# Performance work log

Measured on AMD Instinct MI355X. Metric: run time of the kernel, lower is better.

The kernel has to match this reference:

```python
import jax, jax.numpy as jnp
import numpy as np

B, H, N, D = 4, 8, 4096, 64
F = 64  # nb_features; must equal D because the original code multiplies k_prime (..f) elementwise with v (..d)


def setup_inputs() -> dict:
    key = jax.random.key(0)
    kq, kk, kv, kp = jax.random.split(key, 4)
    # scale inputs so exp(x @ proj.T) stays in fp32 range
    q = jax.random.normal(kq, (B, H, N, D), dtype=jnp.float32) * 0.05
    k = jax.random.normal(kk, (B, H, N, D), dtype=jnp.float32) * 0.05
    v = jax.random.normal(kv, (B, H, N, D), dtype=jnp.float32)
    proj = jax.random.normal(kp, (F, D), dtype=jnp.float32)
    return {"q": q, "k": k, "v": v, "proj": proj}


def reference(q, k, v, proj):
    # exp-kernel feature map: [b,h,n,d] x [f,d] -> [b,h,n,f]
    q_prime = jnp.exp(jnp.einsum('bhnd,fd->bhnf', q, proj))
    k_prime = jnp.exp(jnp.einsum('bhnd,fd->bhnf', k, proj))
    # denominator: sum_f q_prime * (sum_n k_prime + eps) -> [b,h,n]
    k_sum = k_prime.sum(axis=2) + 1e-6                      # [b,h,f]
    d_inv = 1.0 / jnp.einsum('bhnf,bhf->bhn', q_prime, k_sum)
    # context: elementwise product summed over sequence (requires f == d)
    ctx = (k_prime * v).sum(axis=2)                         # [b,h,d]
    out = q_prime * ctx[:, :, None, :] * d_inv[..., None]   # [b,h,n,d]
    return out
```

## Files before the change

kernel.cpp:

```cpp
#include <hip/hip_runtime.h>
#include <hip/hip_bf16.h>


#define NHEADS 32
#define SEQ    4096
#define DDIM   64

typedef __attribute__((ext_vector_type(8))) short short8;
typedef __attribute__((ext_vector_type(4))) float floatx4;

__device__ __forceinline__ short f2bf(float x) {
    unsigned int u = __float_as_uint(x);
    u += 0x7fffu + ((u >> 16) & 1u);
    return (short)(u >> 16);
}

__device__ __forceinline__ short8 load8_bf16(const float* __restrict__ p) {
    floatx4 a = *(const floatx4*)p;
    floatx4 b = *(const floatx4*)(p + 4);
    short8 t;
    t[0] = f2bf(a[0]); t[1] = f2bf(a[1]); t[2] = f2bf(a[2]); t[3] = f2bf(a[3]);
    t[4] = f2bf(b[0]); t[5] = f2bf(b[1]); t[6] = f2bf(b[2]); t[7] = f2bf(b[3]);
    return t;
}

__device__ __forceinline__ void load_bfrag(const float* __restrict__ proj,
                                           int fp, int g, short8 bfrag[4][2]) {
#pragma unroll
    for (int ft = 0; ft < 4; ++ft)
#pragma unroll
        for (int half = 0; half < 2; ++half)
            bfrag[ft][half] = load8_bf16(proj + (ft * 16 + fp) * DDIM + half * 32 + g * 8);
}

__global__ __launch_bounds__(256) void fa_pass1(const float* __restrict__ K,
                                                const float* __restrict__ V,
                                                const float* __restrict__ proj,
                                                float* __restrict__ ws) {
    const int head = blockIdx.x >> 4;
    const int seg  = blockIdx.x & 15;
    const int tid  = threadIdx.x;
    const int w    = tid >> 6;
    const int lane = tid & 63;
    const int fp   = lane & 15;
    const int g    = lane >> 4;

    short8 bfrag[4][2];
    load_bfrag(proj, fp, g, bfrag);

    float ksum[4] = {0.f, 0.f, 0.f, 0.f};
    float ctx[4]  = {0.f, 0.f, 0.f, 0.f};

    const long hbase = (long)head * SEQ;

#pragma unroll
    for (int it = 0; it < 4; ++it) {
        const int row0 = seg * 256 + it * 64 + w * 16;
        const float* ap = K + (hbase + row0 + fp) * DDIM;
        short8 afrag0 = load8_bf16(ap + g * 8);
        short8 afrag1 = load8_bf16(ap + 32 + g * 8);

        floatx4 acc[4];
#pragma unroll
        for (int ft = 0; ft < 4; ++ft) {
            floatx4 z = {0.f, 0.f, 0.f, 0.f};
            z = __builtin_amdgcn_mfma_f32_16x16x32_bf16(afrag0, bfrag[ft][0], z, 0, 0, 0);
            z = __builtin_amdgcn_mfma_f32_16x16x32_bf16(afrag1, bfrag[ft][1], z, 0, 0, 0);
            acc[ft] = z;
        }

#pragma unroll
        for (int ft = 0; ft < 4; ++ft) {
#pragma unroll
            for (int r = 0; r < 4; ++r) {
                float kp = __expf(acc[ft][r]);
                float vv = V[(hbase + row0 + g * 4 + r) * DDIM + ft * 16 + fp];
                ksum[ft] += kp;
                ctx[ft]  += kp * vv;
            }
        }
    }

#pragma unroll
    for (int ft = 0; ft < 4; ++ft) {
        ksum[ft] += __shfl_xor(ksum[ft], 16); ksum[ft] += __shfl_xor(ksum[ft], 32);
        ctx[ft]  += __shfl_xor(ctx[ft], 16);  ctx[ft]  += __shfl_xor(ctx[ft], 32);
    }

    __shared__ float red[4][128];
    if (lane < 16) {
#pragma unroll
        for (int ft = 0; ft < 4; ++ft) {
            red[w][ft * 16 + fp]      = ksum[ft];
            red[w][64 + ft * 16 + fp] = ctx[ft];
        }
    }
    __syncthreads();
    if (tid < 128) {
        float s = red[0][tid] + red[1][tid] + red[2][tid] + red[3][tid];
        atomicAdd(ws + head * 128 + tid, s);
    }
}

__global__ __launch_bounds__(256) void fa_pass2(const float* __restrict__ Q,
                                                const float* __restrict__ proj,
                                                const float* __restrict__ ws,
                                                float* __restrict__ out) {
    const int head = blockIdx.x >> 6;
    const int seg  = blockIdx.x & 63;
    const int tid  = threadIdx.x;
    const int w    = tid >> 6;
    const int lane = tid & 63;
    const int fp   = lane & 15;
    const int g    = lane >> 4;

    short8 bfrag[4][2];
    load_bfrag(proj, fp, g, bfrag);

    float ksr[4], ctxr[4];
#pragma unroll
    for (int ft = 0; ft < 4; ++ft) {
        ksr[ft]  = ws[head * 128 + ft * 16 + fp] + 1e-6f;
        ctxr[ft] = ws[head * 128 + 64 + ft * 16 + fp];
    }

    const long hbase = (long)head * SEQ;
    const int row0 = seg * 64 + w * 16;
    const float* ap = Q + (hbase + row0 + fp) * DDIM;
    short8 afrag0 = load8_bf16(ap + g * 8);
    short8 afrag1 = load8_bf16(ap + 32 + g * 8);

    float qp[4][4];
    float denom[4] = {0.f, 0.f, 0.f, 0.f};
#pragma unroll
    for (int ft = 0; ft < 4; ++ft) {
        floatx4 z = {0.f, 0.f, 0.f, 0.f};
        z = __builtin_amdgcn_mfma_f32_16x16x32_bf16(afrag0, bfrag[ft][0], z, 0, 0, 0);
        z = __builtin_amdgcn_mfma_f32_16x16x32_bf16(afrag1, bfrag[ft][1], z, 0, 0, 0);
#pragma unroll
        for (int r = 0; r < 4; ++r) {
            float e = __expf(z[r]);
            qp[ft][r] = e;
            denom[r] += e * ksr[ft];
        }
    }

#pragma unroll
    for (int r = 0; r < 4; ++r) {
        denom[r] += __shfl_xor(denom[r], 1);
        denom[r] += __shfl_xor(denom[r], 2);
        denom[r] += __shfl_xor(denom[r], 4);
        denom[r] += __shfl_xor(denom[r], 8);
        denom[r] = 1.0f / denom[r];
    }

#pragma unroll
    for (int ft = 0; ft < 4; ++ft)
#pragma unroll
        for (int r = 0; r < 4; ++r)
            out[(hbase + row0 + g * 4 + r) * DDIM + ft * 16 + fp] =
                qp[ft][r] * ctxr[ft] * denom[r];
}

extern "C" void kernel_launch(void* const* d_in, const int* in_sizes, int n_in,
                              void* d_out, int out_size, void* d_ws, size_t ws_size,
                              hipStream_t stream) {
    const float* q    = (const float*)d_in[0];
    const float* k    = (const float*)d_in[1];
    const float* v    = (const float*)d_in[2];
    const float* proj = (const float*)d_in[3];
    float* out = (float*)d_out;
    float* ws  = (float*)d_ws;

    hipMemsetAsync(ws, 0, NHEADS * 128 * sizeof(float), stream);
    fa_pass1<<<NHEADS * 16, 256, 0, stream>>>(k, v, proj, ws);
    fa_pass2<<<NHEADS * 64, 256, 0, stream>>>(q, proj, ws, out);
}
```

Baseline: 149.6 us.

## Precompute bf16 proj fragments in prep kernel and double pass1 grid

Replaces the hipMemsetAsync with a small prep kernel that zeroes the accumulators and also packs proj into bf16 MFMA B-fragment layout in the workspace. Pass1 and pass2 then load their fragments with one vector load each instead of loading fp32 and converting per block. Pass1 launches twice as many blocks, each covering half the sequence rows, for more parallelism at the cost of twice as many atomics. An extra kernel launch is added in place of the memset.

```diff
diff --git a/kernel.cpp b/kernel.cpp
--- a/kernel.cpp
+++ b/kernel.cpp
@@ -5,6 +5,7 @@
 #define NHEADS 32
 #define SEQ    4096
 #define DDIM   64
+#define ACC_FLOATS (NHEADS * 128)
 
 typedef __attribute__((ext_vector_type(8))) short short8;
 typedef __attribute__((ext_vector_type(4))) float floatx4;
@@ -24,29 +25,52 @@
     return t;
 }
 
-__device__ __forceinline__ void load_bfrag(const float* __restrict__ proj,
-                                           int fp, int g, short8 bfrag[4][2]) {
+__device__ __forceinline__ void load_bfrag_ws(const short* __restrict__ pbf,
+                                              int lane, short8 bfrag[4][2]) {
 #pragma unroll
     for (int ft = 0; ft < 4; ++ft)
 #pragma unroll
         for (int half = 0; half < 2; ++half)
-            bfrag[ft][half] = load8_bf16(proj + (ft * 16 + fp) * DDIM + half * 32 + g * 8);
+            bfrag[ft][half] = *(const short8*)(pbf + (ft * 2 + half) * 512 + lane * 8);
+}
+
+__global__ __launch_bounds__(128) void fa_prep(const float* __restrict__ proj,
+                                               float* __restrict__ ws) {
+    const int tid = threadIdx.x;
+    if (blockIdx.x < 32) {
+        ws[blockIdx.x * 128 + tid] = 0.0f;
+        return;
+    }
+    short* pbf = (short*)(ws + ACC_FLOATS);
+#pragma unroll
+    for (int i = 0; i < 32; ++i) {
+        int idx  = tid * 32 + i;
+        int ft2h = idx >> 9;
+        int rem  = idx & 511;
+        int lane = rem >> 3;
+        int j    = rem & 7;
+        int ft   = ft2h >> 1;
+        int half = ft2h & 1;
+        int fp   = lane & 15;
+        int g    = lane >> 4;
+        pbf[idx] = f2bf(proj[(ft * 16 + fp) * DDIM + half * 32 + g * 8 + j]);
+    }
 }
 
 __global__ __launch_bounds__(256) void fa_pass1(const float* __restrict__ K,
                                                 const float* __restrict__ V,
-                                                const float* __restrict__ proj,
                                                 float* __restrict__ ws) {
-    const int head = blockIdx.x >> 4;
-    const int seg  = blockIdx.x & 15;
+    const int head = blockIdx.x >> 5;
+    const int seg  = blockIdx.x & 31;
     const int tid  = threadIdx.x;
     const int w    = tid >> 6;
     const int lane = tid & 63;
     const int fp   = lane & 15;
     const int g    = lane >> 4;
 
+    const short* pbf = (const short*)(ws + ACC_FLOATS);
     short8 bfrag[4][2];
-    load_bfrag(proj, fp, g, bfrag);
+    load_bfrag_ws(pbf, lane, bfrag);
 
     float ksum[4] = {0.f, 0.f, 0.f, 0.f};
     float ctx[4]  = {0.f, 0.f, 0.f, 0.f};
@@ -54,8 +78,8 @@
     const long hbase = (long)head * SEQ;
 
 #pragma unroll
-    for (int it = 0; it < 4; ++it) {
-        const int row0 = seg * 256 + it * 64 + w * 16;
+    for (int it = 0; it < 2; ++it) {
+        const int row0 = seg * 128 + it * 64 + w * 16;
         const float* ap = K + (hbase + row0 + fp) * DDIM;
         short8 afrag0 = load8_bf16(ap + g * 8);
         short8 afrag1 = load8_bf16(ap + 32 + g * 8);
@@ -103,7 +127,6 @@
 }
 
 __global__ __launch_bounds__(256) void fa_pass2(const float* __restrict__ Q,
-                                                const float* __restrict__ proj,
                                                 const float* __restrict__ ws,
                                                 float* __restrict__ out) {
     const int head = blockIdx.x >> 6;
@@ -114,8 +137,9 @@
     const int fp   = lane & 15;
     const int g    = lane >> 4;
 
+    const short* pbf = (const short*)(ws + ACC_FLOATS);
     short8 bfrag[4][2];
-    load_bfrag(proj, fp, g, bfrag);
+    load_bfrag_ws(pbf, lane, bfrag);
 
     float ksr[4], ctxr[4];
 #pragma unroll
@@ -172,7 +196,7 @@
     float* out = (float*)d_out;
     float* ws  = (float*)d_ws;
 
-    hipMemsetAsync(ws, 0, NHEADS * 128 * sizeof(float), stream);
-    fa_pass1<<<NHEADS * 16, 256, 0, stream>>>(k, v, proj, ws);
-    fa_pass2<<<NHEADS * 64, 256, 0, stream>>>(q, proj, ws, out);
-}
+    fa_prep<<<33, 128, 0, stream>>>(proj, ws);
+    fa_pass1<<<NHEADS * 32, 256, 0, stream>>>(k, v, ws);
+    fa_pass2<<<NHEADS * 64, 256, 0, stream>>>(q, ws, out);
+}
```

Result: faster. 139.6 us (-6.6%).

## Drop memset and atomics, permute features for vectorized V/out access, use exp2

Applied to the files above, without the earlier changes.

Pass 1 now writes per-block partial sums to the workspace and pass 2 reduces them, which removes the memset launch and the global atomics. The feature index mapping is permuted (fp*4+ft) so V loads and output stores become 16-byte vector accesses instead of scalar strided ones. Exp is computed with the exp2 intrinsic on log2e-prescaled projection weights. Grid sizes change and pass 2 now handles 128 rows per block, adding a small redundant partial-sum reduction in every block.

```diff
diff --git a/kernel.cpp b/kernel.cpp
--- a/kernel.cpp
+++ b/kernel.cpp
@@ -1,13 +1,14 @@
 #include <hip/hip_runtime.h>
-#include <hip/hip_bf16.h>
 
 
 #define NHEADS 32
 #define SEQ    4096
 #define DDIM   64
+#define LOG2E  1.44269504088896341f
 
 typedef __attribute__((ext_vector_type(8))) short short8;
 typedef __attribute__((ext_vector_type(4))) float floatx4;
+typedef __attribute__((ext_vector_type(2))) float floatx2;
 
 __device__ __forceinline__ short f2bf(float x) {
     unsigned int u = __float_as_uint(x);
@@ -24,59 +25,69 @@
     return t;
 }
 
-__device__ __forceinline__ void load_bfrag(const float* __restrict__ proj,
+__device__ __forceinline__ short8 load8_bf16_scale(const float* __restrict__ p, float s) {
+    floatx4 a = *(const floatx4*)p;
+    floatx4 b = *(const floatx4*)(p + 4);
+    short8 t;
+    t[0] = f2bf(a[0] * s); t[1] = f2bf(a[1] * s); t[2] = f2bf(a[2] * s); t[3] = f2bf(a[3] * s);
+    t[4] = f2bf(b[0] * s); t[5] = f2bf(b[1] * s); t[6] = f2bf(b[2] * s); t[7] = f2bf(b[3] * s);
+    return t;
+}
+
+__device__ __forceinline__ void make_bfrag(const float* __restrict__ proj,
                                            int fp, int g, short8 bfrag[4][2]) {
 #pragma unroll
     for (int ft = 0; ft < 4; ++ft)
 #pragma unroll
         for (int half = 0; half < 2; ++half)
-            bfrag[ft][half] = load8_bf16(proj + (ft * 16 + fp) * DDIM + half * 32 + g * 8);
-}
-
-__global__ __launch_bounds__(256) void fa_pass1(const float* __restrict__ K,
-                                                const float* __restrict__ V,
-                                                const float* __restrict__ proj,
-                                                float* __restrict__ ws) {
-    const int head = blockIdx.x >> 4;
-    const int seg  = blockIdx.x & 15;
+            bfrag[ft][half] =
+                load8_bf16_scale(proj + (fp * 4 + ft) * DDIM + half * 32 + g * 8, LOG2E);
+}
+
+__global__ __launch_bounds__(256, 4) void fa_pass1(const float* __restrict__ K,
+                                                   const float* __restrict__ V,
+                                                   const float* __restrict__ proj,
+                                                   float* __restrict__ ws) {
+    const int bid  = blockIdx.x;
+    const int head = bid >> 5;
+    const int seg  = bid & 31;
     const int tid  = threadIdx.x;
     const int w    = tid >> 6;
     const int lane = tid & 63;
     const int fp   = lane & 15;
     const int g    = lane >> 4;
+    const long hbase = (long)head * SEQ;
 
     short8 bfrag[4][2];
-    load_bfrag(proj, fp, g, bfrag);
+    make_bfrag(proj, fp, g, bfrag);
 
     float ksum[4] = {0.f, 0.f, 0.f, 0.f};
     float ctx[4]  = {0.f, 0.f, 0.f, 0.f};
 
-    const long hbase = (long)head * SEQ;
-
-#pragma unroll
-    for (int it = 0; it < 4; ++it) {
-        const int row0 = seg * 256 + it * 64 + w * 16;
+#pragma unroll
+    for (int it = 0; it < 2; ++it) {
+        const int row0 = seg * 128 + it * 64 + w * 16;
         const float* ap = K + (hbase + row0 + fp) * DDIM;
-        short8 afrag0 = load8_bf16(ap + g * 8);
-        short8 afrag1 = load8_bf16(ap + 32 + g * 8);
+        short8 a0 = load8_bf16(ap + g * 8);
+        short8 a1 = load8_bf16(ap + 32 + g * 8);
 
         floatx4 acc[4];
 #pragma unroll
         for (int ft = 0; ft < 4; ++ft) {
             floatx4 z = {0.f, 0.f, 0.f, 0.f};
-            z = __builtin_amdgcn_mfma_f32_16x16x32_bf16(afrag0, bfrag[ft][0], z, 0, 0, 0);
-            z = __builtin_amdgcn_mfma_f32_16x16x32_bf16(afrag1, bfrag[ft][1], z, 0, 0, 0);
+            z = __builtin_amdgcn_mfma_f32_16x16x32_bf16(a0, bfrag[ft][0], z, 0, 0, 0);
+            z = __builtin_amdgcn_mfma_f32_16x16x32_bf16(a1, bfrag[ft][1], z, 0, 0, 0);
             acc[ft] = z;
         }
-
-#pragma unroll
-        for (int ft = 0; ft < 4; ++ft) {
-#pragma unroll
-            for (int r = 0; r < 4; ++r) {
-                float kp = __expf(acc[ft][r]);
-                float vv = V[(hbase + row0 + g * 4 + r) * DDIM + ft * 16 + fp];
+#pragma unroll
+        for (int r = 0; r < 4; ++r) {
+            const floatx4 vv =
+                *(const floatx4*)(V + (hbase + row0 + g * 4 + r) * DDIM + fp * 4);
+#pragma unroll
+            for (int ft = 0; ft < 4; ++ft) {
+                float kp = __builtin_amdgcn_exp2f(acc[ft][r]);
                 ksum[ft] += kp;
-                ctx[ft]  += kp * vv;
+                ctx[ft]  += kp * vv[ft];
             }
         }
     }
@@ -86,80 +97,97 @@
         ksum[ft] += __shfl_xor(ksum[ft], 16); ksum[ft] += __shfl_xor(ksum[ft], 32);
         ctx[ft]  += __shfl_xor(ctx[ft], 16);  ctx[ft]  += __shfl_xor(ctx[ft], 32);
     }
-
-    __shared__ float red[4][128];
+    __shared__ float smem[4][128];
     if (lane < 16) {
 #pragma unroll
         for (int ft = 0; ft < 4; ++ft) {
-            red[w][ft * 16 + fp]      = ksum[ft];
-            red[w][64 + ft * 16 + fp] = ctx[ft];
+            smem[w][fp * 4 + ft]      = ksum[ft];
+            smem[w][64 + fp * 4 + ft] = ctx[ft];
         }
     }
     __syncthreads();
-    if (tid < 128) {
-        float s = red[0][tid] + red[1][tid] + red[2][tid] + red[3][tid];
-        atomicAdd(ws + head * 128 + tid, s);
-    }
-}
-
-__global__ __launch_bounds__(256) void fa_pass2(const float* __restrict__ Q,
-                                                const float* __restrict__ proj,
-                                                const float* __restrict__ ws,
-                                                float* __restrict__ out) {
-    const int head = blockIdx.x >> 6;
-    const int seg  = blockIdx.x & 63;
+    if (tid < 128)
+        ws[bid * 128 + tid] = smem[0][tid] + smem[1][tid] + smem[2][tid] + smem[3][tid];
+}
+
+__global__ __launch_bounds__(256, 4) void fa_pass2(const float* __restrict__ Q,
+                                                   const float* __restrict__ proj,
+                                                   const float* __restrict__ ws,
+                                                   float* __restrict__ out) {
+    const int bid  = blockIdx.x;
+    const int head = bid >> 5;
+    const int seg  = bid & 31;
     const int tid  = threadIdx.x;
     const int w    = tid >> 6;
     const int lane = tid & 63;
     const int fp   = lane & 15;
     const int g    = lane >> 4;
+    const long hbase = (long)head * SEQ;
+
+    short8 qfrag[2][2];
+#pragma unroll
+    for (int it = 0; it < 2; ++it) {
+        const float* qp_ = Q + (hbase + seg * 128 + it * 64 + w * 16 + fp) * DDIM;
+        qfrag[it][0] = load8_bf16(qp_ + g * 8);
+        qfrag[it][1] = load8_bf16(qp_ + 32 + g * 8);
+    }
 
     short8 bfrag[4][2];
-    load_bfrag(proj, fp, g, bfrag);
-
-    float ksr[4], ctxr[4];
-#pragma unroll
-    for (int ft = 0; ft < 4; ++ft) {
-        ksr[ft]  = ws[head * 128 + ft * 16 + fp] + 1e-6f;
-        ctxr[ft] = ws[head * 128 + 64 + ft * 16 + fp];
-    }
-
-    const long hbase = (long)head * SEQ;
-    const int row0 = seg * 64 + w * 16;
-    const float* ap = Q + (hbase + row0 + fp) * DDIM;
-    short8 afrag0 = load8_bf16(ap + g * 8);
-    short8 afrag1 = load8_bf16(ap + 32 + g * 8);
-
-    float qp[4][4];
-    float denom[4] = {0.f, 0.f, 0.f, 0.f};
-#pragma unroll
-    for (int ft = 0; ft < 4; ++ft) {
-        floatx4 z = {0.f, 0.f, 0.f, 0.f};
-        z = __builtin_amdgcn_mfma_f32_16x16x32_bf16(afrag0, bfrag[ft][0], z, 0, 0, 0);
-        z = __builtin_amdgcn_mfma_f32_16x16x32_bf16(afrag1, bfrag[ft][1], z, 0, 0, 0);
+    make_bfrag(proj, fp, g, bfrag);
+
+    floatx2 acc2 = {0.f, 0.f};
+#pragma unroll
+    for (int p = 0; p < 8; ++p) {
+        floatx2 t = *(const floatx2*)(ws + (long)(head * 32 + w * 8 + p) * 128 + lane * 2);
+        acc2[0] += t[0];
+        acc2[1] += t[1];
+    }
+    __shared__ float smem[4][128];
+    smem[w][lane * 2]     = acc2[0];
+    smem[w][lane * 2 + 1] = acc2[1];
+    __syncthreads();
+    if (tid < 128)
+        smem[0][tid] = smem[0][tid] + smem[1][tid] + smem[2][tid] + smem[3][tid];
+    __syncthreads();
+    floatx4 ksr  = *(const floatx4*)(&smem[0][fp * 4]);
+    floatx4 ctxr = *(const floatx4*)(&smem[0][64 + fp * 4]);
+#pragma unroll
+    for (int ft = 0; ft < 4; ++ft) ksr[ft] += 1e-6f;
+
+#pragma unroll
+    for (int it = 0; it < 2; ++it) {
+        const int row0 = seg * 128 + it * 64 + w * 16;
+        float qp[4][4];
+        float denom[4] = {0.f, 0.f, 0.f, 0.f};
+#pragma unroll
+        for (int ft = 0; ft < 4; ++ft) {
+            floatx4 z = {0.f, 0.f, 0.f, 0.f};
+            z = __builtin_amdgcn_mfma_f32_16x16x32_bf16(qfrag[it][0], bfrag[ft][0], z, 0, 0, 0);
+            z = __builtin_amdgcn_mfma_f32_16x16x32_bf16(qfrag[it][1], bfrag[ft][1], z, 0, 0, 0);
+#pragma unroll
+            for (int r = 0; r < 4; ++r) {
+                float e = __builtin_amdgcn_exp2f(z[r]);
+                qp[ft][r] = e;
+                denom[r] += e * ksr[ft];
+            }
+        }
 #pragma unroll
         for (int r = 0; r < 4; ++r) {
-            float e = __expf(z[r]);
-            qp[ft][r] = e;
-            denom[r] += e * ksr[ft];
-        }
-    }
-
-#pragma unroll
-    for (int r = 0; r < 4; ++r) {
-        denom[r] += __shfl_xor(denom[r], 1);
-        denom[r] += __shfl_xor(denom[r], 2);
-        denom[r] += __shfl_xor(denom[r], 4);
-        denom[r] += __shfl_xor(denom[r], 8);
-        denom[r] = 1.0f / denom[r];
-    }
-
-#pragma unroll
-    for (int ft = 0; ft < 4; ++ft)
-#pragma unroll
-        for (int r = 0; r < 4; ++r)
-            out[(hbase + row0 + g * 4 + r) * DDIM + ft * 16 + fp] =
-                qp[ft][r] * ctxr[ft] * denom[r];
+            denom[r] += __shfl_xor(denom[r], 1);
+            denom[r] += __shfl_xor(denom[r], 2);
+            denom[r] += __shfl_xor(denom[r], 4);
+            denom[r] += __shfl_xor(denom[r], 8);
+            denom[r] = 1.0f / denom[r];
+        }
+#pragma unroll
+        for (int r = 0; r < 4; ++r) {
+            floatx4 o;
+#pragma unroll
+            for (int ft = 0; ft < 4; ++ft)
+                o[ft] = qp[ft][r] * ctxr[ft] * denom[r];
+            *(floatx4*)(out + (hbase + row0 + g * 4 + r) * DDIM + fp * 4) = o;
+        }
+    }
 }
 
 extern "C" void kernel_launch(void* const* d_in, const int* in_sizes, int n_in,
@@ -172,7 +200,6 @@
     float* out = (float*)d_out;
     float* ws  = (float*)d_ws;
 
-    hipMemsetAsync(ws, 0, NHEADS * 128 * sizeof(float), stream);
-    fa_pass1<<<NHEADS * 16, 256, 0, stream>>>(k, v, proj, ws);
-    fa_pass2<<<NHEADS * 64, 256, 0, stream>>>(q, proj, ws, out);
-}
+    fa_pass1<<<NHEADS * 32, 256, 0, stream>>>(k, v, proj, ws);
+    fa_pass2<<<NHEADS * 32, 256, 0, stream>>>(q, proj, ws, out);
+}
```

After: 144.0 us. 1.04x faster.
